# Kernel optimization log

Measured on AMD Instinct MI355X. Metric: run time of the kernel, lower is better.

## Reference

```python
import jax, jax.numpy as jnp
import numpy as np

LN_EPS = 1e-5


def _layernorm(x, w, b):
    mu = jnp.mean(x, axis=-1, keepdims=True)
    var = jnp.mean(jnp.square(x - mu), axis=-1, keepdims=True)
    return (x - mu) * jax.lax.rsqrt(var + LN_EPS) * w + b


def setup_inputs() -> dict:
    key = jax.random.key(0)
    ks = jax.random.split(key, 6)
    B, V, P, D = 32, 4, 784, 768
    H = 8
    x = jax.random.normal(ks[0], (B, V * P, D), dtype=jnp.float32)
    s = 0.02  # init scale for weights
    return {
        "x": x,
        "num_views": V,
        "norm1_w": jnp.ones((D,), jnp.float32),
        "norm1_b": jnp.zeros((D,), jnp.float32),
        "in_proj_w": jax.random.normal(ks[1], (3 * D, D), jnp.float32) * s,
        "in_proj_b": jnp.zeros((3 * D,), jnp.float32),
        "out_w": jax.random.normal(ks[2], (D, D), jnp.float32) * s,
        "out_b": jnp.zeros((D,), jnp.float32),
        "norm2_w": jnp.ones((D,), jnp.float32),
        "norm2_b": jnp.zeros((D,), jnp.float32),
        "ffn_w1": jax.random.normal(ks[3], (4 * D, D), jnp.float32) * s,
        "ffn_b1": jnp.zeros((4 * D,), jnp.float32),
        "ffn_w2": jax.random.normal(ks[4], (D, 4 * D), jnp.float32) * s,
        "ffn_b2": jnp.zeros((D,), jnp.float32),
    }


def reference(x, num_views, norm1_w, norm1_b, in_proj_w, in_proj_b, out_w, out_b,
              norm2_w, norm2_b, ffn_w1, ffn_b1, ffn_w2, ffn_b2):
    B, T, D = x.shape
    V = num_views
    P = T // V
    H = 8
    dh = D // H

    # The per-patch python loop in the original is embarrassingly parallel over
    # patches: fold the patch dim into batch -> (B*P, V, D) tokens of seq-len V.
    xv = x.reshape(B, V, P, D).transpose(0, 2, 1, 3).reshape(B * P, V, D)

    # pre-norm cross-view attention (torch MultiheadAttention, batch_first)
    h = _layernorm(xv, norm1_w, norm1_b)
    qkv = h @ in_proj_w.T + in_proj_b                      # (BP, V, 3D)
    q, k, v = jnp.split(qkv, 3, axis=-1)
    q = q.reshape(B * P, V, H, dh).transpose(0, 2, 1, 3)   # (BP, H, V, dh)
    k = k.reshape(B * P, V, H, dh).transpose(0, 2, 1, 3)
    v = v.reshape(B * P, V, H, dh).transpose(0, 2, 1, 3)
    scores = jnp.einsum("bhqd,bhkd->bhqk", q, k) / jnp.sqrt(jnp.float32(dh))
    attn = jax.nn.softmax(scores, axis=-1)
    o = jnp.einsum("bhqk,bhkd->bhqd", attn, v)             # (BP, H, V, dh)
    o = o.transpose(0, 2, 1, 3).reshape(B * P, V, D)
    o = o @ out_w.T + out_b
    xv = xv + o

    # pre-norm FFN with exact (erf) GELU; dropout = identity (eval mode)
    h = _layernorm(xv, norm2_w, norm2_b)
    h = jax.nn.gelu(h @ ffn_w1.T + ffn_b1, approximate=False)
    xv = xv + (h @ ffn_w2.T + ffn_b2)

    # undo the fold: (BP, V, D) -> (B, P, V, D) -> (B, V, P, D) -> (B, T, D)
    return xv.reshape(B, P, V, D).transpose(0, 2, 1, 3).reshape(B, T, D)
```

## Files before the change

### kernel.cpp

```cpp
#include <hip/hip_runtime.h>
#include <hip/hip_bf16.h>
#include <math.h>

typedef __bf16 bf16x8 __attribute__((ext_vector_type(8)));
typedef float  f32x4  __attribute__((ext_vector_type(4)));
typedef unsigned short us8 __attribute__((ext_vector_type(8)));
typedef unsigned short us4 __attribute__((ext_vector_type(4)));
typedef unsigned short ush;

__device__ __forceinline__ unsigned short f2bf(float x) {
  unsigned int u = __float_as_uint(x);
  u += 0x7FFFu + ((u >> 16) & 1u);
  return (unsigned short)(u >> 16);
}
__device__ __forceinline__ float bf2f(unsigned short v) {
  return __uint_as_float(((unsigned int)v) << 16);
}
__device__ __forceinline__ float gelu_t(float x) {
  float y = 0.7978845608028654f * x * (1.0f + 0.044715f * x * x);
  float e = __expf(2.0f * y);
  return x - x / (e + 1.0f);
}


__global__ __launch_bounds__(256) void conv_f32_bf16(const float* __restrict__ s,
                                                     unsigned short* __restrict__ d, int n4) {
  int i = blockIdx.x * 256 + threadIdx.x;
  if (i >= n4) return;
  float4 f = ((const float4*)s)[i];
  ushort4 u;
  u.x = f2bf(f.x); u.y = f2bf(f.y); u.z = f2bf(f.z); u.w = f2bf(f.w);
  ((ushort4*)d)[i] = u;
}

__global__ __launch_bounds__(256) void ln_kernel(const float* __restrict__ src,
                                                 const float* __restrict__ w,
                                                 const float* __restrict__ b,
                                                 unsigned short* __restrict__ dst) {
  const int wv = threadIdx.x >> 6;
  const int lane = threadIdx.x & 63;
  const int n = blockIdx.x * 4 + wv;
  const int bp = n >> 2, v = n & 3;
  const int bb = bp / 784, p = bp - bb * 784;
  const float* row = src + ((size_t)bb * 3136 + (size_t)v * 784 + p) * 768;
  float4 x0 = ((const float4*)row)[lane];
  float4 x1 = ((const float4*)row)[lane + 64];
  float4 x2 = ((const float4*)row)[lane + 128];
  float s  = x0.x + x0.y + x0.z + x0.w + x1.x + x1.y + x1.z + x1.w
           + x2.x + x2.y + x2.z + x2.w;
  float ss = x0.x*x0.x + x0.y*x0.y + x0.z*x0.z + x0.w*x0.w
           + x1.x*x1.x + x1.y*x1.y + x1.z*x1.z + x1.w*x1.w
           + x2.x*x2.x + x2.y*x2.y + x2.z*x2.z + x2.w*x2.w;
  #pragma unroll
  for (int off = 32; off > 0; off >>= 1) {
    s  += __shfl_xor(s,  off, 64);
    ss += __shfl_xor(ss, off, 64);
  }
  const float mu   = s * (1.0f / 768.0f);
  const float rstd = rsqrtf(ss * (1.0f / 768.0f) - mu * mu + 1e-5f);
  const int r = n & 255;
  unsigned short* bb2 = dst + (((size_t)(n >> 8) * 12) << 14) + r * 64
                      + ((((lane >> 1) & 7) ^ (r & 7)) << 3) + ((lane & 1) << 2);
  #pragma unroll
  for (int seg = 0; seg < 3; ++seg) {
    float4 xs = (seg == 0) ? x0 : (seg == 1) ? x1 : x2;
    float4 w4 = ((const float4*)w)[lane + seg * 64];
    float4 b4 = ((const float4*)b)[lane + seg * 64];
    us4 u;
    u[0] = f2bf((xs.x - mu) * rstd * w4.x + b4.x);
    u[1] = f2bf((xs.y - mu) * rstd * w4.y + b4.y);
    u[2] = f2bf((xs.z - mu) * rstd * w4.z + b4.z);
    u[3] = f2bf((xs.w - mu) * rstd * w4.w + b4.w);
    *(us4*)(bb2 + (((size_t)((lane >> 4) + seg * 4)) << 14)) = u;
  }
}


#define BARX() do { asm volatile("" ::: "memory"); \
                    __builtin_amdgcn_s_barrier();  \
                    asm volatile("" ::: "memory"); } while (0)
#define WAITVM(N) asm volatile("s_waitcnt vmcnt(" #N ")" ::: "memory")

#define STAGE_A(HALF, TT) do {                                                \
  _Pragma("unroll")                                                           \
  for (int _j = 0; _j < 2; ++_j) {                                            \
    const int _ob = ((HALF) << 13) + (w << 10) + (_j << 9);                   \
    __builtin_amdgcn_global_load_lds(                                         \
        (const __attribute__((address_space(1))) void*)(                      \
            gAt + (((size_t)(TT)) << 14) + _ob + lnoff8),                     \
        (__attribute__((address_space(3))) void*)(                            \
            smem + ((((TT) & 1)) << 15) + _ob), 16, 0, 0);                    \
  }                                                                           \
} while (0)

#define STAGE_B(HALF, TT) do {                                                \
  const int _l0 = ((((TT) & 1)) << 15) + 16384 + ((HALF) << 13) + (w << 9);   \
  const ush* _g = gB + (size_t)(((HALF) << 7) + (w << 3)) * K                 \
                + (((size_t)(TT)) << 6);                                      \
  __builtin_amdgcn_global_load_lds(                                           \
      (const __attribute__((address_space(1))) void*)_g,                      \
      (__attribute__((address_space(3))) void*)(smem + _l0), 16, 0, 0);       \
  __builtin_amdgcn_global_load_lds(                                           \
      (const __attribute__((address_space(1))) void*)(_g + ((size_t)K << 6)), \
      (__attribute__((address_space(3))) void*)(smem + _l0 + 4096), 16, 0, 0);\
} while (0)

#define LDA(HM) do {                                                          \
  _Pragma("unroll")                                                           \
  for (int mi4 = 0; mi4 < 4; ++mi4) {                                         \
    const int m = wm * 64 + (HM) * 128 + mi4 * 16 + l16;                      \
    _Pragma("unroll")                                                         \
    for (int kk = 0; kk < 2; ++kk) {                                          \
      const int q = kk * 4 + quad;                                            \
      af[mi4][kk] = *(const bf16x8*)(smem + aofs + m * 64 + ((q ^ (m & 7)) << 3)); \
    }                                                                         \
  }                                                                           \
} while (0)

#define LDB(HN, BF) do {                                                      \
  _Pragma("unroll")                                                           \
  for (int ni2 = 0; ni2 < 2; ++ni2) {                                         \
    const int n = wn * 32 + (HN) * 128 + ni2 * 16 + l16;                      \
    _Pragma("unroll")                                                         \
    for (int kk = 0; kk < 2; ++kk) {                                          \
      const int q = kk * 4 + quad;                                            \
      BF[ni2][kk] = *(const bf16x8*)(smem + bofs + n * 64 + ((q ^ (n & 7)) << 3)); \
    }                                                                         \
  }                                                                           \
} while (0)

#define MFMAC(HM, HN, BF) do {                                                \
  __builtin_amdgcn_s_setprio(1);                                              \
  _Pragma("unroll")                                                           \
  for (int mi4 = 0; mi4 < 4; ++mi4)                                           \
    _Pragma("unroll")                                                         \
    for (int ni2 = 0; ni2 < 2; ++ni2)                                         \
      _Pragma("unroll")                                                       \
      for (int kk = 0; kk < 2; ++kk)                                          \
        acc[(HM)*4 + mi4][(HN)*2 + ni2] = __builtin_amdgcn_mfma_f32_16x16x32_bf16( \
            af[mi4][kk], BF[ni2][kk], acc[(HM)*4 + mi4][(HN)*2 + ni2], 0, 0, 0); \
  __builtin_amdgcn_s_setprio(0);                                              \
} while (0)

template <int K, int EPI>
__global__ __launch_bounds__(512, 2) void gemm256(const ush* __restrict__ A,
                                                  const ush* __restrict__ Bm,
                                                  const float* __restrict__ bias,
                                                  void* __restrict__ outp,
                                                  const float* __restrict__ aux,
                                                  int N) {
  __shared__ __attribute__((aligned(16))) ush smem[65536];
  constexpr int NT = K / 64;
  const int tid  = threadIdx.x;
  const int w    = tid >> 6;
  const int lane = tid & 63;
  const int quad = lane >> 4;
  const int l16  = lane & 15;
  const int wm   = w >> 2;
  const int wn   = w & 3;

  const int gx   = gridDim.x;
  const int nwg  = gx * 392;
  const int flat = blockIdx.y * gx + blockIdx.x;
  const int xcd  = flat & 7;
  const int pos  = xcd * (nwg >> 3) + (flat >> 3);
  const int by   = pos / gx;
  const int bx   = pos - by * gx;

  const ush* gAt   = A + (((size_t)by * NT) << 14);
  const int  lnoff8 = lane << 3;

  const int r8  = lane >> 3;
  const int cb  = lane & 7;
  const int swo = (cb ^ r8) << 3;
  const ush* gB = Bm + (size_t)(bx * 256 + r8) * K + swo;

  f32x4 acc[8][4];
  #pragma unroll
  for (int i = 0; i < 8; ++i)
    #pragma unroll
    for (int j = 0; j < 4; ++j) {
      f32x4 z = {0.0f, 0.0f, 0.0f, 0.0f};
      acc[i][j] = z;
    }
  bf16x8 af[4][2], bf0[2][2], bf1[2][2];

  STAGE_A(0, 0); STAGE_B(0, 0); STAGE_A(1, 0);
  STAGE_B(1, 0); STAGE_A(0, 1); STAGE_B(0, 1);
  WAITVM(8);
  BARX();

  #pragma unroll 2
  for (int t = 0; t < NT; ++t) {
    const int aofs = (t & 1) << 15;
    const int bofs = aofs + 16384;
    LDA(0); LDB(0, bf0);
    if (t <= NT - 2) STAGE_A(1, t + 1);
    BARX();
    MFMAC(0, 0, bf0);
    if (t < NT - 1) { WAITVM(6); } else { WAITVM(0); }
    BARX();
    LDB(1, bf1);
    if (t <= NT - 2) STAGE_B(1, t + 1);
    BARX();
    MFMAC(0, 1, bf1);
    BARX();
    LDA(1);
    if (t <= NT - 3) STAGE_A(0, t + 2);
    BARX();
    MFMAC(1, 0, bf0);
    BARX();
    if (t <= NT - 3) STAGE_B(0, t + 2);
    BARX();
    MFMAC(1, 1, bf1);
    if (t <= NT - 3)      { WAITVM(8); }
    else if (t == NT - 2) { WAITVM(4); }
    BARX();
  }

  float* lsm = (float*)smem;
  #pragma unroll
  for (int s = 0; s < 4; ++s) {
    if (wm == (s & 1)) {
      const int hm = s >> 1;
      #pragma unroll
      for (int mi4 = 0; mi4 < 4; ++mi4)
        #pragma unroll
        for (int ni = 0; ni < 4; ++ni) {
          const int col = wn * 32 + (ni >> 1) * 128 + (ni & 1) * 16 + l16;
          #pragma unroll
          for (int r = 0; r < 4; ++r) {
            const int row_l = mi4 * 16 + quad * 4 + r;
            lsm[row_l * 260 + col] = acc[hm * 4 + mi4][ni][r];
          }
        }
    }
    __syncthreads();
    #pragma unroll
    for (int j = 0; j < 8; ++j) {
      const int cc    = tid + 512 * j;
      const int row_l = cc >> 6;
      const int c4    = (cc & 63) << 2;
      f32x4 vv = *(const f32x4*)&lsm[row_l * 260 + c4];
      const int rr    = by * 256 + s * 64 + row_l;
      const int col_g = bx * 256 + c4;
      f32x4 b4 = *(const f32x4*)&bias[col_g];
      vv += b4;
      if (EPI == 0) {
        const int seg = col_g / 768;
        const int c2  = col_g - seg * 768;
        const int hh  = c2 / 96;
        const int dd  = c2 - hh * 96;
        const int bp = rr >> 2, v = rr & 3;
        us4 u = { f2bf(vv[0]), f2bf(vv[1]), f2bf(vv[2]), f2bf(vv[3]) };
        *(us4*)((unsigned short*)outp + (size_t)bp * 9216 + seg * 3072 + hh * 384 + v * 96 + dd) = u;
      } else if (EPI == 1 || EPI == 3) {
        const int bp = rr >> 2, v = rr & 3;
        const int bb = bp / 784, p = bp - bb * 784;
        const size_t addr = ((size_t)bb * 3136 + (size_t)v * 784 + p) * 768 + col_g;
        f32x4 a4 = *(const f32x4*)(aux + addr);
        vv += a4;
        *(f32x4*)((float*)outp + addr) = vv;
      } else {
        us4 u = { f2bf(gelu_t(vv[0])), f2bf(gelu_t(vv[1])),
                  f2bf(gelu_t(vv[2])), f2bf(gelu_t(vv[3])) };
        const int rb = rr & 255;
        *(us4*)((unsigned short*)outp
               + (((size_t)(rr >> 8) * 48 + (col_g >> 6)) << 14)
               + rb * 64 + ((((col_g >> 3) & 7) ^ (rb & 7)) << 3) + (col_g & 7)) = u;
      }
    }
    __syncthreads();
  }
}

__global__ __launch_bounds__(256) void attn_kernel(const unsigned short* __restrict__ qs,
                                                   unsigned short* __restrict__ o) {
  int idx = blockIdx.x * 256 + threadIdx.x;
  int vq = idx & 3;
  int h  = (idx >> 2) & 7;
  int bp = idx >> 5;
  const unsigned short* qp = qs + (size_t)bp * 9216 + h * 384 + vq * 96;
  const unsigned short* kp = qs + (size_t)bp * 9216 + 3072 + h * 384;
  const unsigned short* vp = qs + (size_t)bp * 9216 + 6144 + h * 384;
  float s0 = 0.f, s1 = 0.f, s2 = 0.f, s3 = 0.f;
  #pragma unroll
  for (int c = 0; c < 96; c += 8) {
    us8 q8 = *(const us8*)(qp + c);
    us8 k0 = *(const us8*)(kp + c);
    us8 k1 = *(const us8*)(kp + 96 + c);
    us8 k2 = *(const us8*)(kp + 192 + c);
    us8 k3 = *(const us8*)(kp + 288 + c);
    #pragma unroll
    for (int j = 0; j < 8; ++j) {
      float qf = bf2f(q8[j]);
      s0 += qf * bf2f(k0[j]);
      s1 += qf * bf2f(k1[j]);
      s2 += qf * bf2f(k2[j]);
      s3 += qf * bf2f(k3[j]);
    }
  }
  const float scale = 0.10206207261596575f;
  s0 *= scale; s1 *= scale; s2 *= scale; s3 *= scale;
  float m = fmaxf(fmaxf(s0, s1), fmaxf(s2, s3));
  float e0 = __expf(s0 - m), e1 = __expf(s1 - m), e2 = __expf(s2 - m), e3 = __expf(s3 - m);
  float inv = 1.0f / (e0 + e1 + e2 + e3);
  e0 *= inv; e1 *= inv; e2 *= inv; e3 *= inv;
  const int rn = bp * 4 + vq;
  const int rr2 = rn & 255;
  unsigned short* ob = o + (((size_t)(rn >> 8) * 12) << 14) + rr2 * 64;
  #pragma unroll
  for (int c = 0; c < 96; c += 8) {
    us8 v0 = *(const us8*)(vp + c);
    us8 v1 = *(const us8*)(vp + 96 + c);
    us8 v2 = *(const us8*)(vp + 192 + c);
    us8 v3 = *(const us8*)(vp + 288 + c);
    us8 r;
    #pragma unroll
    for (int j = 0; j < 8; ++j) {
      float val = e0 * bf2f(v0[j]) + e1 * bf2f(v1[j]) + e2 * bf2f(v2[j]) + e3 * bf2f(v3[j]);
      r[j] = f2bf(val);
    }
    const int k = h * 96 + c;
    *(us8*)(ob + (((size_t)(k >> 6)) << 14) + ((((k >> 3) & 7) ^ (rr2 & 7)) << 3)) = r;
  }
}

extern "C" void kernel_launch(void* const* d_in, const int* in_sizes, int n_in,
                              void* d_out, int out_size, void* d_ws, size_t ws_size,
                              hipStream_t stream) {
  const float* x         = (const float*)d_in[0];
  const float* norm1_w   = (const float*)d_in[2];
  const float* norm1_b   = (const float*)d_in[3];
  const float* in_proj_w = (const float*)d_in[4];
  const float* in_proj_b = (const float*)d_in[5];
  const float* out_w     = (const float*)d_in[6];
  const float* out_b     = (const float*)d_in[7];
  const float* norm2_w   = (const float*)d_in[8];
  const float* norm2_b   = (const float*)d_in[9];
  const float* ffn_w1    = (const float*)d_in[10];
  const float* ffn_b1    = (const float*)d_in[11];
  const float* ffn_w2    = (const float*)d_in[12];
  const float* ffn_b2    = (const float*)d_in[13];
  float* out = (float*)d_out;

  char* ws = (char*)d_ws;
  unsigned short* wq = (unsigned short*)ws;
  unsigned short* wh = (unsigned short*)(ws + 616562688u);
  unsigned short* wB = (unsigned short*)(ws + 616562688u + 154140672u);
  unsigned short* wIn  = wB;
  unsigned short* wOut = wB + 1769472;
  unsigned short* wF1  = wOut + 589824;
  unsigned short* wF2  = wF1 + 2359296;

  conv_f32_bf16<<<(442368 + 255) / 256, 256, 0, stream>>>(in_proj_w, wIn, 442368);
  conv_f32_bf16<<<(147456 + 255) / 256, 256, 0, stream>>>(out_w, wOut, 147456);
  conv_f32_bf16<<<(589824 + 255) / 256, 256, 0, stream>>>(ffn_w1, wF1, 589824);
  conv_f32_bf16<<<(589824 + 255) / 256, 256, 0, stream>>>(ffn_w2, wF2, 589824);

  ln_kernel<<<25088, 256, 0, stream>>>(x, norm1_w, norm1_b, wh);
  gemm256<768, 0><<<dim3(9, 392), 512, 0, stream>>>(wh, wIn, in_proj_b, (void*)wq, nullptr, 2304);
  attn_kernel<<<3136, 256, 0, stream>>>(wq, wh);
  gemm256<768, 1><<<dim3(3, 392), 512, 0, stream>>>(wh, wOut, out_b, (void*)out, x, 768);
  ln_kernel<<<25088, 256, 0, stream>>>(out, norm2_w, norm2_b, wh);
  gemm256<768, 2><<<dim3(12, 392), 512, 0, stream>>>(wh, wF1, ffn_b1, (void*)wq, nullptr, 3072);
  gemm256<3072, 3><<<dim3(3, 392), 512, 0, stream>>>(wq, wF2, ffn_b2, (void*)out, out, 768);

  (void)in_sizes; (void)n_in; (void)out_size; (void)ws_size;
}
```

Before: 2.691 ms.

## Add grouped tile raster per XCD, nontemporal streaming accesses, cheaper GELU formula

Reorders the workgroup-to-tile mapping in the GEMM so each XCD works on a contiguous band of row tiles, grouped by GB column tiles, to improve L2 reuse of A and B. Marks single-use streaming loads and stores (LN input, attention qkv reads, epilogue outputs) as nontemporal so they pollute the cache less. Rewrites the tanh-GELU as a single exp2 and hardware reciprocal with folded constants. The nontemporal hints could hurt if data is reused soon, such as the residual stream read back by the second LN.

```diff
diff --git a/kernel.cpp b/kernel.cpp
--- a/kernel.cpp
+++ b/kernel.cpp
@@ -17,9 +17,9 @@
   return __uint_as_float(((unsigned int)v) << 16);
 }
 __device__ __forceinline__ float gelu_t(float x) {
-  float y = 0.7978845608028654f * x * (1.0f + 0.044715f * x * x);
-  float e = __expf(2.0f * y);
-  return x - x / (e + 1.0f);
+  float s = 2.30220897f + 0.10294325f * x * x;
+  float t = __builtin_amdgcn_exp2f(-x * s);
+  return x * __builtin_amdgcn_rcpf(1.0f + t);
 }
 
 
@@ -27,10 +27,10 @@
                                                      unsigned short* __restrict__ d, int n4) {
   int i = blockIdx.x * 256 + threadIdx.x;
   if (i >= n4) return;
-  float4 f = ((const float4*)s)[i];
-  ushort4 u;
-  u.x = f2bf(f.x); u.y = f2bf(f.y); u.z = f2bf(f.z); u.w = f2bf(f.w);
-  ((ushort4*)d)[i] = u;
+  f32x4 f = ((const f32x4*)s)[i];
+  us4 u;
+  u[0] = f2bf(f[0]); u[1] = f2bf(f[1]); u[2] = f2bf(f[2]); u[3] = f2bf(f[3]);
+  ((us4*)d)[i] = u;
 }
 
 __global__ __launch_bounds__(256) void ln_kernel(const float* __restrict__ src,
@@ -43,14 +43,14 @@
   const int bp = n >> 2, v = n & 3;
   const int bb = bp / 784, p = bp - bb * 784;
   const float* row = src + ((size_t)bb * 3136 + (size_t)v * 784 + p) * 768;
-  float4 x0 = ((const float4*)row)[lane];
-  float4 x1 = ((const float4*)row)[lane + 64];
-  float4 x2 = ((const float4*)row)[lane + 128];
-  float s  = x0.x + x0.y + x0.z + x0.w + x1.x + x1.y + x1.z + x1.w
-           + x2.x + x2.y + x2.z + x2.w;
-  float ss = x0.x*x0.x + x0.y*x0.y + x0.z*x0.z + x0.w*x0.w
-           + x1.x*x1.x + x1.y*x1.y + x1.z*x1.z + x1.w*x1.w
-           + x2.x*x2.x + x2.y*x2.y + x2.z*x2.z + x2.w*x2.w;
+  f32x4 x0 = __builtin_nontemporal_load((const f32x4*)row + lane);
+  f32x4 x1 = __builtin_nontemporal_load((const f32x4*)row + lane + 64);
+  f32x4 x2 = __builtin_nontemporal_load((const f32x4*)row + lane + 128);
+  float s  = x0[0] + x0[1] + x0[2] + x0[3] + x1[0] + x1[1] + x1[2] + x1[3]
+           + x2[0] + x2[1] + x2[2] + x2[3];
+  float ss = x0[0]*x0[0] + x0[1]*x0[1] + x0[2]*x0[2] + x0[3]*x0[3]
+           + x1[0]*x1[0] + x1[1]*x1[1] + x1[2]*x1[2] + x1[3]*x1[3]
+           + x2[0]*x2[0] + x2[1]*x2[1] + x2[2]*x2[2] + x2[3]*x2[3];
   #pragma unroll
   for (int off = 32; off > 0; off >>= 1) {
     s  += __shfl_xor(s,  off, 64);
@@ -63,14 +63,14 @@
                       + ((((lane >> 1) & 7) ^ (r & 7)) << 3) + ((lane & 1) << 2);
   #pragma unroll
   for (int seg = 0; seg < 3; ++seg) {
-    float4 xs = (seg == 0) ? x0 : (seg == 1) ? x1 : x2;
-    float4 w4 = ((const float4*)w)[lane + seg * 64];
-    float4 b4 = ((const float4*)b)[lane + seg * 64];
+    f32x4 xs = (seg == 0) ? x0 : (seg == 1) ? x1 : x2;
+    f32x4 w4 = ((const f32x4*)w)[lane + seg * 64];
+    f32x4 b4 = ((const f32x4*)b)[lane + seg * 64];
     us4 u;
-    u[0] = f2bf((xs.x - mu) * rstd * w4.x + b4.x);
-    u[1] = f2bf((xs.y - mu) * rstd * w4.y + b4.y);
-    u[2] = f2bf((xs.z - mu) * rstd * w4.z + b4.z);
-    u[3] = f2bf((xs.w - mu) * rstd * w4.w + b4.w);
+    u[0] = f2bf((xs[0] - mu) * rstd * w4[0] + b4[0]);
+    u[1] = f2bf((xs[1] - mu) * rstd * w4[1] + b4[1]);
+    u[2] = f2bf((xs[2] - mu) * rstd * w4[2] + b4[2]);
+    u[3] = f2bf((xs[3] - mu) * rstd * w4[3] + b4[3]);
     *(us4*)(bb2 + (((size_t)((lane >> 4) + seg * 4)) << 14)) = u;
   }
 }
@@ -148,7 +148,7 @@
                                                   const float* __restrict__ bias,
                                                   void* __restrict__ outp,
                                                   const float* __restrict__ aux,
-                                                  int N) {
+                                                  int N, int GB) {
   __shared__ __attribute__((aligned(16))) ush smem[65536];
   constexpr int NT = K / 64;
   const int tid  = threadIdx.x;
@@ -160,12 +160,15 @@
   const int wn   = w & 3;
 
   const int gx   = gridDim.x;
-  const int nwg  = gx * 392;
   const int flat = blockIdx.y * gx + blockIdx.x;
   const int xcd  = flat & 7;
-  const int pos  = xcd * (nwg >> 3) + (flat >> 3);
-  const int by   = pos / gx;
-  const int bx   = pos - by * gx;
+  const int p    = flat >> 3;
+  const int gsz  = GB * 49;
+  const int g    = p / gsz;
+  const int r    = p - g * gsz;
+  const int byo  = r / GB;
+  const int by   = xcd * 49 + byo;
+  const int bx   = g * GB + (r - byo * GB);
 
   const ush* gAt   = A + (((size_t)by * NT) << 14);
   const int  lnoff8 = lane << 3;
@@ -229,9 +232,9 @@
         for (int ni = 0; ni < 4; ++ni) {
           const int col = wn * 32 + (ni >> 1) * 128 + (ni & 1) * 16 + l16;
           #pragma unroll
-          for (int r = 0; r < 4; ++r) {
-            const int row_l = mi4 * 16 + quad * 4 + r;
-            lsm[row_l * 260 + col] = acc[hm * 4 + mi4][ni][r];
+          for (int r2 = 0; r2 < 4; ++r2) {
+            const int row_l = mi4 * 16 + quad * 4 + r2;
+            lsm[row_l * 260 + col] = acc[hm * 4 + mi4][ni][r2];
           }
         }
     }
@@ -253,21 +256,26 @@
         const int dd  = c2 - hh * 96;
         const int bp = rr >> 2, v = rr & 3;
         us4 u = { f2bf(vv[0]), f2bf(vv[1]), f2bf(vv[2]), f2bf(vv[3]) };
-        *(us4*)((unsigned short*)outp + (size_t)bp * 9216 + seg * 3072 + hh * 384 + v * 96 + dd) = u;
+        __builtin_nontemporal_store(u,
+            (us4*)((unsigned short*)outp + (size_t)bp * 9216 + seg * 3072 + hh * 384 + v * 96 + dd));
       } else if (EPI == 1 || EPI == 3) {
         const int bp = rr >> 2, v = rr & 3;
-        const int bb = bp / 784, p = bp - bb * 784;
-        const size_t addr = ((size_t)bb * 3136 + (size_t)v * 784 + p) * 768 + col_g;
-        f32x4 a4 = *(const f32x4*)(aux + addr);
+        const int bb = bp / 784, p2 = bp - bb * 784;
+        const size_t addr = ((size_t)bb * 3136 + (size_t)v * 784 + p2) * 768 + col_g;
+        f32x4 a4;
+        if (EPI == 1) a4 = __builtin_nontemporal_load((const f32x4*)(aux + addr));
+        else          a4 = *(const f32x4*)(aux + addr);
         vv += a4;
-        *(f32x4*)((float*)outp + addr) = vv;
+        if (EPI == 1) *(f32x4*)((float*)outp + addr) = vv;
+        else __builtin_nontemporal_store(vv, (f32x4*)((float*)outp + addr));
       } else {
         us4 u = { f2bf(gelu_t(vv[0])), f2bf(gelu_t(vv[1])),
                   f2bf(gelu_t(vv[2])), f2bf(gelu_t(vv[3])) };
         const int rb = rr & 255;
-        *(us4*)((unsigned short*)outp
+        __builtin_nontemporal_store(u,
+            (us4*)((unsigned short*)outp
                + (((size_t)(rr >> 8) * 48 + (col_g >> 6)) << 14)
-               + rb * 64 + ((((col_g >> 3) & 7) ^ (rb & 7)) << 3) + (col_g & 7)) = u;
+               + rb * 64 + ((((col_g >> 3) & 7) ^ (rb & 7)) << 3) + (col_g & 7)));
       }
     }
     __syncthreads();
@@ -286,11 +294,11 @@
   float s0 = 0.f, s1 = 0.f, s2 = 0.f, s3 = 0.f;
   #pragma unroll
   for (int c = 0; c < 96; c += 8) {
-    us8 q8 = *(const us8*)(qp + c);
-    us8 k0 = *(const us8*)(kp + c);
-    us8 k1 = *(const us8*)(kp + 96 + c);
-    us8 k2 = *(const us8*)(kp + 192 + c);
-    us8 k3 = *(const us8*)(kp + 288 + c);
+    us8 q8 = __builtin_nontemporal_load((const us8*)(qp + c));
+    us8 k0 = __builtin_nontemporal_load((const us8*)(kp + c));
+    us8 k1 = __builtin_nontemporal_load((const us8*)(kp + 96 + c));
+    us8 k2 = __builtin_nontemporal_load((const us8*)(kp + 192 + c));
+    us8 k3 = __builtin_nontemporal_load((const us8*)(kp + 288 + c));
     #pragma unroll
     for (int j = 0; j < 8; ++j) {
       float qf = bf2f(q8[j]);
@@ -311,10 +319,10 @@
   unsigned short* ob = o + (((size_t)(rn >> 8) * 12) << 14) + rr2 * 64;
   #pragma unroll
   for (int c = 0; c < 96; c += 8) {
-    us8 v0 = *(const us8*)(vp + c);
-    us8 v1 = *(const us8*)(vp + 96 + c);
-    us8 v2 = *(const us8*)(vp + 192 + c);
-    us8 v3 = *(const us8*)(vp + 288 + c);
+    us8 v0 = __builtin_nontemporal_load((const us8*)(vp + c));
+    us8 v1 = __builtin_nontemporal_load((const us8*)(vp + 96 + c));
+    us8 v2 = __builtin_nontemporal_load((const us8*)(vp + 192 + c));
+    us8 v3 = __builtin_nontemporal_load((const us8*)(vp + 288 + c));
     us8 r;
     #pragma unroll
     for (int j = 0; j < 8; ++j) {
@@ -359,12 +367,12 @@
   conv_f32_bf16<<<(589824 + 255) / 256, 256, 0, stream>>>(ffn_w2, wF2, 589824);
 
   ln_kernel<<<25088, 256, 0, stream>>>(x, norm1_w, norm1_b, wh);
-  gemm256<768, 0><<<dim3(9, 392), 512, 0, stream>>>(wh, wIn, in_proj_b, (void*)wq, nullptr, 2304);
+  gemm256<768, 0><<<dim3(9, 392), 512, 0, stream>>>(wh, wIn, in_proj_b, (void*)wq, nullptr, 2304, 3);
   attn_kernel<<<3136, 256, 0, stream>>>(wq, wh);
-  gemm256<768, 1><<<dim3(3, 392), 512, 0, stream>>>(wh, wOut, out_b, (void*)out, x, 768);
+  gemm256<768, 1><<<dim3(3, 392), 512, 0, stream>>>(wh, wOut, out_b, (void*)out, x, 768, 3);
   ln_kernel<<<25088, 256, 0, stream>>>(out, norm2_w, norm2_b, wh);
-  gemm256<768, 2><<<dim3(12, 392), 512, 0, stream>>>(wh, wF1, ffn_b1, (void*)wq, nullptr, 3072);
-  gemm256<3072, 3><<<dim3(3, 392), 512, 0, stream>>>(wq, wF2, ffn_b2, (void*)out, out, 768);
+  gemm256<768, 2><<<dim3(12, 392), 512, 0, stream>>>(wh, wF1, ffn_b1, (void*)wq, nullptr, 3072, 4);
+  gemm256<3072, 3><<<dim3(3, 392), 512, 0, stream>>>(wq, wF2, ffn_b2, (void*)out, out, 768, 3);
 
   (void)in_sizes; (void)n_in; (void)out_size; (void)ws_size;
 }
```

After: 2.754 ms. +2.4%, slower.
